# Kernel optimization log

Hardware: AMD Instinct MI355X
Metric: run time of the kernel (lower is better)

## Reference

```python
import jax, jax.numpy as jnp
import numpy as np
from jax import lax

DT = 0.001            # Euler step_size (forward default)
STEPS_PER_OUT = 5     # t spacing 0.005 / dt 0.001 (t grid aligned with step grid)


def setup_inputs() -> dict:
    key = jax.random.key(0)
    ks = jax.random.split(key, 6)
    B, K, C, F, H = 8192, 2, 2, 64, 64
    D = C * F
    x0 = jax.random.normal(ks[0], (B, K, C, F), dtype=jnp.float32)
    t = jnp.arange(51, dtype=jnp.float32) * 0.005  # 51 output times, aligned to dt grid
    # Kaiming-ish small init so tanh stays in a sane range over 250 Euler steps
    W1 = jax.random.normal(ks[1], (D, H), dtype=jnp.float32) / jnp.sqrt(jnp.float32(D))
    b1 = jax.random.normal(ks[2], (H,), dtype=jnp.float32) * 0.01
    W2 = jax.random.normal(ks[3], (H, D), dtype=jnp.float32) / jnp.sqrt(jnp.float32(H))
    b2 = jax.random.normal(ks[4], (D,), dtype=jnp.float32) * 0.01
    return {"x0": x0, "t": t, "W1": W1, "b1": b1, "W2": W2, "b2": b2}


def reference(x0, t, W1, b1, W2, b2):
    B, K, C, F = x0.shape
    T = t.shape[0]

    def dydt(y):  # tiny 2-layer tanh MLP derivative, y: [B, C*F]
        return jnp.tanh(y @ W1 + b1) @ W2 + b2

    def euler_substep(i, y):
        return y + DT * dydt(y)

    def interval(y, _):
        # STEPS_PER_OUT fixed Euler steps between consecutive output times
        y = lax.fori_loop(0, STEPS_PER_OUT, euler_substep, y)
        return y, y

    y0 = x0.reshape(B, K, C * F)[:, 0]            # flatten(start_dim=-2) then [:, 0]
    _, ys = lax.scan(interval, y0, None, length=T - 1)  # [T-1, B, D]
    out = jnp.concatenate([y0[None], ys], axis=0)       # [T, B, D]
    out = jnp.transpose(out, (1, 0, 2))                 # permute(1,0,2) -> [B, T, D]
    return out.reshape(B, T, C, F)                      # unflatten -> [B, T, C, F]
```

## Files before the change

### kernel.cpp

```cpp
#include <hip/hip_runtime.h>
#include <hip/hip_bf16.h>


typedef __attribute__((ext_vector_type(8))) short bf16x8;
typedef __attribute__((ext_vector_type(4))) float floatx4;

__device__ float g_w21[64 * 64 + 64];

static __device__ __forceinline__ short f2bf(float f) {
    return __builtin_bit_cast(short, (__bf16)f);
}

static __device__ __forceinline__ unsigned pack2(float a, float b) {
    unsigned short lo = __builtin_bit_cast(unsigned short, (__bf16)a);
    unsigned short hi = __builtin_bit_cast(unsigned short, (__bf16)b);
    return (unsigned)lo | ((unsigned)hi << 16);
}

static __device__ __forceinline__ float tanh_fast(float x) {
    float e = __expf(2.0f * x);
    return 1.0f - 2.0f * __builtin_amdgcn_rcpf(1.0f + e);
}

__global__ __launch_bounds__(64) void precompute_kernel(
    const float* __restrict__ W1, const float* __restrict__ W2,
    const float* __restrict__ b2)
{
    const int hout = threadIdx.x;
    const int hin  = blockIdx.x;
    float a0 = 0.f, a1 = 0.f, a2 = 0.f, a3 = 0.f;
    if (hin < 64) {
        #pragma unroll 4
        for (int d = 0; d < 128; d += 4) {
            a0 = fmaf(W2[hin * 128 + d + 0], W1[(d + 0) * 64 + hout], a0);
            a1 = fmaf(W2[hin * 128 + d + 1], W1[(d + 1) * 64 + hout], a1);
            a2 = fmaf(W2[hin * 128 + d + 2], W1[(d + 2) * 64 + hout], a2);
            a3 = fmaf(W2[hin * 128 + d + 3], W1[(d + 3) * 64 + hout], a3);
        }
        g_w21[hin * 64 + hout] = (a0 + a1) + (a2 + a3);
    } else {
        #pragma unroll 4
        for (int d = 0; d < 128; d += 4) {
            a0 = fmaf(b2[d + 0], W1[(d + 0) * 64 + hout], a0);
            a1 = fmaf(b2[d + 1], W1[(d + 1) * 64 + hout], a1);
            a2 = fmaf(b2[d + 2], W1[(d + 2) * 64 + hout], a2);
            a3 = fmaf(b2[d + 3], W1[(d + 3) * 64 + hout], a3);
        }
        g_w21[4096 + hout] = (a0 + a1) + (a2 + a3);
    }
}

__global__ __launch_bounds__(256, 1) void node_kernel(
    const float* __restrict__ x0, const float* __restrict__ W1,
    const float* __restrict__ b1, const float* __restrict__ W2,
    const float* __restrict__ b2, float* __restrict__ out)
{
    __shared__ __align__(16) unsigned short Ald[2][16 * 64];
    __shared__ __align__(16) unsigned short Sld[16 * 64];
    __shared__ __align__(16) unsigned short Yld[16 * 128];

    const int tid  = threadIdx.x;
    const int w    = tid >> 6;
    const int lane = tid & 63;
    const int n    = lane & 15;
    const int q    = lane >> 4;
    const int row  = (blockIdx.x << 4) + n;
    const int swz  = n & 7;

    bf16x8 w21f[2];
    #pragma unroll
    for (int kt = 0; kt < 2; ++kt) {
        const int m  = w * 16 + n;
        const int k0 = kt * 32 + q * 8;
        bf16x8 v;
        #pragma unroll
        for (int j = 0; j < 8; ++j) v[j] = f2bf(g_w21[(k0 + j) * 64 + m]);
        w21f[kt] = v;
    }
    bf16x8 w2f[2][2];
    #pragma unroll
    for (int i = 0; i < 2; ++i) {
        #pragma unroll
        for (int kt = 0; kt < 2; ++kt) {
            const int m  = w * 32 + i * 16 + n;
            const int k0 = kt * 32 + q * 8;
            bf16x8 v;
            #pragma unroll
            for (int j = 0; j < 8; ++j) v[j] = f2bf(W2[(k0 + j) * 128 + m]);
            w2f[i][kt] = v;
        }
    }

    floatx4 cf, b1f, b2f5[2];
    #pragma unroll
    for (int r = 0; r < 4; ++r) {
        cf[r]  = g_w21[4096 + w * 16 + q * 4 + r];
        b1f[r] = b1[w * 16 + q * 4 + r];
    }
    #pragma unroll
    for (int i = 0; i < 2; ++i)
        #pragma unroll
        for (int r = 0; r < 4; ++r)
            b2f5[i][r] = 5.0f * b2[w * 32 + i * 16 + q * 4 + r];

    floatx4 y[2];
    #pragma unroll
    for (int i = 0; i < 2; ++i)
        #pragma unroll
        for (int r = 0; r < 4; ++r)
            y[i][r] = x0[row * 256 + w * 32 + i * 16 + q * 4 + r];

    #pragma unroll
    for (int i = 0; i < 2; ++i) {
        const int j0 = 4 * w + 2 * i + (q >> 1);
        uint2 p;
        p.x = pack2(y[i][0], y[i][1]);
        p.y = pack2(y[i][2], y[i][3]);
        *reinterpret_cast<uint2*>(&Yld[n * 128 + (j0 ^ swz) * 8 + (q & 1) * 4]) = p;
        *reinterpret_cast<floatx4*>(out + row * 51 * 128 + w * 32 + i * 16 + q * 4) = y[i];
    }
    __syncthreads();

    floatx4 z = b1f;
    #pragma unroll
    for (int kt = 0; kt < 4; ++kt) {
        bf16x8 yb = __builtin_bit_cast(bf16x8, *reinterpret_cast<const uint4*>(
            &Yld[n * 128 + ((kt * 4 + q) ^ swz) * 8]));
        const int m  = w * 16 + n;
        const int k0 = kt * 32 + q * 8;
        bf16x8 w1t;
        #pragma unroll
        for (int j = 0; j < 8; ++j) w1t[j] = f2bf(W1[(k0 + j) * 64 + m]);
        z = __builtin_amdgcn_mfma_f32_16x16x32_bf16(w1t, yb, z, 0, 0, 0);
    }

    floatx4 S = {0.0f, 0.0f, 0.0f, 0.0f};

    const int awr  = n * 64 + (((2 * w + (q >> 1)) ^ swz) * 8) + (q & 1) * 4;
    const int ard0 = n * 64 + ((q ^ swz) * 8);
    const int ard1 = n * 64 + (((4 + q) ^ swz) * 8);

    for (int ti = 1; ti <= 50; ++ti) {
        #pragma unroll
        for (int ss = 0; ss < 5; ++ss) {
            const int p = ss & 1;
            float a0 = tanh_fast(z[0]);
            float a1 = tanh_fast(z[1]);
            float a2 = tanh_fast(z[2]);
            float a3 = tanh_fast(z[3]);
            S[0] += a0; S[1] += a1; S[2] += a2; S[3] += a3;
            uint2 pa;
            pa.x = pack2(a0, a1);
            pa.y = pack2(a2, a3);
            *reinterpret_cast<uint2*>(&Ald[p][awr]) = pa;
            if (ss == 4) {
                uint2 ps;
                ps.x = pack2(S[0], S[1]);
                ps.y = pack2(S[2], S[3]);
                *reinterpret_cast<uint2*>(&Sld[awr]) = ps;
            }
            __syncthreads();

            bf16x8 ab0 = __builtin_bit_cast(bf16x8,
                *reinterpret_cast<const uint4*>(&Ald[p][ard0]));
            bf16x8 ab1 = __builtin_bit_cast(bf16x8,
                *reinterpret_cast<const uint4*>(&Ald[p][ard1]));
            floatx4 acc = cf;
            acc = __builtin_amdgcn_mfma_f32_16x16x32_bf16(w21f[0], ab0, acc, 0, 0, 0);
            acc = __builtin_amdgcn_mfma_f32_16x16x32_bf16(w21f[1], ab1, acc, 0, 0, 0);
            #pragma unroll
            for (int r = 0; r < 4; ++r) z[r] = fmaf(0.001f, acc[r], z[r]);

            if (ss == 4) {
                bf16x8 sb0 = __builtin_bit_cast(bf16x8,
                    *reinterpret_cast<const uint4*>(&Sld[ard0]));
                bf16x8 sb1 = __builtin_bit_cast(bf16x8,
                    *reinterpret_cast<const uint4*>(&Sld[ard1]));
                floatx4 acc2[2] = { b2f5[0], b2f5[1] };
                #pragma unroll
                for (int i = 0; i < 2; ++i) {
                    acc2[i] = __builtin_amdgcn_mfma_f32_16x16x32_bf16(
                        w2f[i][0], sb0, acc2[i], 0, 0, 0);
                    acc2[i] = __builtin_amdgcn_mfma_f32_16x16x32_bf16(
                        w2f[i][1], sb1, acc2[i], 0, 0, 0);
                }
                #pragma unroll
                for (int i = 0; i < 2; ++i) {
                    #pragma unroll
                    for (int r = 0; r < 4; ++r)
                        y[i][r] = fmaf(0.001f, acc2[i][r], y[i][r]);
                    *reinterpret_cast<floatx4*>(
                        out + row * 51 * 128 + ti * 128 + w * 32 + i * 16 + q * 4) = y[i];
                }
                S = floatx4{0.0f, 0.0f, 0.0f, 0.0f};
                __syncthreads();
            }
        }
    }
}

extern "C" void kernel_launch(void* const* d_in, const int* in_sizes, int n_in,
                              void* d_out, int out_size, void* d_ws, size_t ws_size,
                              hipStream_t stream) {
    const float* x0 = (const float*)d_in[0];
    const float* W1 = (const float*)d_in[2];
    const float* b1 = (const float*)d_in[3];
    const float* W2 = (const float*)d_in[4];
    const float* b2 = (const float*)d_in[5];
    float* out = (float*)d_out;

    precompute_kernel<<<dim3(65), dim3(64), 0, stream>>>(W1, W2, b2);
    node_kernel<<<dim3(512), dim3(256), 0, stream>>>(x0, W1, b1, W2, b2, out);
}
```

Baseline: 262.3 us.

## Collapse each 16-row block to one wavefront to eliminate barrier synchronization

Each block of 16 batch rows is now handled by a single 64-lane wavefront instead of four, so that wave computes all four hidden-unit tiles and all eight output tiles itself. Because the activations are exchanged only within one wavefront, the per-substep __syncthreads calls are removed. W2 fragments are staged once into LDS and read from there per interval instead of being held in registers. The trade-off is 4x more serial MFMA and tanh work per wave and only 512 waves across the whole GPU, which may underuse the compute units. It also relies on LDS ordering within a single wavefront without explicit barriers.

```diff
diff --git a/kernel.cpp b/kernel.cpp
--- a/kernel.cpp
+++ b/kernel.cpp
@@ -50,151 +50,144 @@
     }
 }
 
-__global__ __launch_bounds__(256, 1) void node_kernel(
+__global__ __launch_bounds__(64) void node_kernel(
     const float* __restrict__ x0, const float* __restrict__ W1,
     const float* __restrict__ b1, const float* __restrict__ W2,
     const float* __restrict__ b2, float* __restrict__ out)
 {
-    __shared__ __align__(16) unsigned short Ald[2][16 * 64];
-    __shared__ __align__(16) unsigned short Sld[16 * 64];
-    __shared__ __align__(16) unsigned short Yld[16 * 128];
-
-    const int tid  = threadIdx.x;
-    const int w    = tid >> 6;
-    const int lane = tid & 63;
+    __shared__ __align__(16) unsigned short Trp[16 * 64];
+    __shared__ __align__(16) unsigned short W2f[16 * 64 * 8];
+    __shared__ __align__(16) float B2f[128];
+
+    const int lane = threadIdx.x;
     const int n    = lane & 15;
     const int q    = lane >> 4;
     const int row  = (blockIdx.x << 4) + n;
-    const int swz  = n & 7;
-
-    bf16x8 w21f[2];
-    #pragma unroll
-    for (int kt = 0; kt < 2; ++kt) {
-        const int m  = w * 16 + n;
-        const int k0 = kt * 32 + q * 8;
-        bf16x8 v;
-        #pragma unroll
-        for (int j = 0; j < 8; ++j) v[j] = f2bf(g_w21[(k0 + j) * 64 + m]);
-        w21f[kt] = v;
-    }
-    bf16x8 w2f[2][2];
-    #pragma unroll
-    for (int i = 0; i < 2; ++i) {
+    const int e    = n & 7;
+
+    for (int s = lane; s < 1024; s += 64) {
+        const int f  = s >> 6;
+        const int l  = s & 63;
+        const int k0 = (f & 1) * 32 + (l >> 4) * 8;
+        const int m  = (f >> 1) * 16 + (l & 15);
+        uint4 wv;
+        wv.x = pack2(W2[(k0 + 0) * 128 + m], W2[(k0 + 1) * 128 + m]);
+        wv.y = pack2(W2[(k0 + 2) * 128 + m], W2[(k0 + 3) * 128 + m]);
+        wv.z = pack2(W2[(k0 + 4) * 128 + m], W2[(k0 + 5) * 128 + m]);
+        wv.w = pack2(W2[(k0 + 6) * 128 + m], W2[(k0 + 7) * 128 + m]);
+        *reinterpret_cast<uint4*>(&W2f[s * 8]) = wv;
+    }
+    if (lane < 32) {
+        floatx4 v = *reinterpret_cast<const floatx4*>(&b2[lane * 4]);
+        floatx4 v5 = {5.f * v[0], 5.f * v[1], 5.f * v[2], 5.f * v[3]};
+        *reinterpret_cast<floatx4*>(&B2f[lane * 4]) = v5;
+    }
+
+    bf16x8 w21f[4][2];
+    floatx4 cf[4];
+    #pragma unroll
+    for (int mt = 0; mt < 4; ++mt) {
         #pragma unroll
         for (int kt = 0; kt < 2; ++kt) {
-            const int m  = w * 32 + i * 16 + n;
             const int k0 = kt * 32 + q * 8;
             bf16x8 v;
             #pragma unroll
-            for (int j = 0; j < 8; ++j) v[j] = f2bf(W2[(k0 + j) * 128 + m]);
-            w2f[i][kt] = v;
-        }
-    }
-
-    floatx4 cf, b1f, b2f5[2];
-    #pragma unroll
-    for (int r = 0; r < 4; ++r) {
-        cf[r]  = g_w21[4096 + w * 16 + q * 4 + r];
-        b1f[r] = b1[w * 16 + q * 4 + r];
-    }
-    #pragma unroll
-    for (int i = 0; i < 2; ++i)
-        #pragma unroll
-        for (int r = 0; r < 4; ++r)
-            b2f5[i][r] = 5.0f * b2[w * 32 + i * 16 + q * 4 + r];
-
-    floatx4 y[2];
-    #pragma unroll
-    for (int i = 0; i < 2; ++i)
-        #pragma unroll
-        for (int r = 0; r < 4; ++r)
-            y[i][r] = x0[row * 256 + w * 32 + i * 16 + q * 4 + r];
-
-    #pragma unroll
-    for (int i = 0; i < 2; ++i) {
-        const int j0 = 4 * w + 2 * i + (q >> 1);
-        uint2 p;
-        p.x = pack2(y[i][0], y[i][1]);
-        p.y = pack2(y[i][2], y[i][3]);
-        *reinterpret_cast<uint2*>(&Yld[n * 128 + (j0 ^ swz) * 8 + (q & 1) * 4]) = p;
-        *reinterpret_cast<floatx4*>(out + row * 51 * 128 + w * 32 + i * 16 + q * 4) = y[i];
-    }
-    __syncthreads();
-
-    floatx4 z = b1f;
+            for (int j = 0; j < 8; ++j)
+                v[j] = f2bf(g_w21[(k0 + j) * 64 + mt * 16 + n]);
+            w21f[mt][kt] = v;
+        }
+        cf[mt] = *reinterpret_cast<const floatx4*>(&g_w21[4096 + mt * 16 + q * 4]);
+    }
+
+    floatx4 y[8];
+    float* const outp = out + (size_t)row * (51 * 128);
+    #pragma unroll
+    for (int mt8 = 0; mt8 < 8; ++mt8) {
+        y[mt8] = *reinterpret_cast<const floatx4*>(&x0[row * 256 + mt8 * 16 + q * 4]);
+        *reinterpret_cast<floatx4*>(outp + mt8 * 16 + q * 4) = y[mt8];
+    }
+
+    floatx4 z[4];
+    #pragma unroll
+    for (int mt = 0; mt < 4; ++mt)
+        z[mt] = *reinterpret_cast<const floatx4*>(&b1[mt * 16 + q * 4]);
     #pragma unroll
     for (int kt = 0; kt < 4; ++kt) {
-        bf16x8 yb = __builtin_bit_cast(bf16x8, *reinterpret_cast<const uint4*>(
-            &Yld[n * 128 + ((kt * 4 + q) ^ swz) * 8]));
-        const int m  = w * 16 + n;
-        const int k0 = kt * 32 + q * 8;
-        bf16x8 w1t;
-        #pragma unroll
-        for (int j = 0; j < 8; ++j) w1t[j] = f2bf(W1[(k0 + j) * 64 + m]);
-        z = __builtin_amdgcn_mfma_f32_16x16x32_bf16(w1t, yb, z, 0, 0, 0);
-    }
-
-    floatx4 S = {0.0f, 0.0f, 0.0f, 0.0f};
-
-    const int awr  = n * 64 + (((2 * w + (q >> 1)) ^ swz) * 8) + (q & 1) * 4;
-    const int ard0 = n * 64 + ((q ^ swz) * 8);
-    const int ard1 = n * 64 + (((4 + q) ^ swz) * 8);
+        floatx4 lo = *reinterpret_cast<const floatx4*>(&x0[row * 256 + kt * 32 + q * 8]);
+        floatx4 hi = *reinterpret_cast<const floatx4*>(&x0[row * 256 + kt * 32 + q * 8 + 4]);
+        bf16x8 yb;
+        yb[0] = f2bf(lo[0]); yb[1] = f2bf(lo[1]); yb[2] = f2bf(lo[2]); yb[3] = f2bf(lo[3]);
+        yb[4] = f2bf(hi[0]); yb[5] = f2bf(hi[1]); yb[6] = f2bf(hi[2]); yb[7] = f2bf(hi[3]);
+        #pragma unroll
+        for (int mt = 0; mt < 4; ++mt) {
+            const int k0 = kt * 32 + q * 8;
+            bf16x8 wf;
+            #pragma unroll
+            for (int j = 0; j < 8; ++j)
+                wf[j] = f2bf(W1[(k0 + j) * 64 + mt * 16 + n]);
+            z[mt] = __builtin_amdgcn_mfma_f32_16x16x32_bf16(wf, yb, z[mt], 0, 0, 0);
+        }
+    }
+
+    floatx4 S[4];
+    #pragma unroll
+    for (int mt = 0; mt < 4; ++mt) S[mt] = floatx4{0.f, 0.f, 0.f, 0.f};
+
+    char* const trp = reinterpret_cast<char*>(Trp);
+    int wr[4], rd[2];
+    #pragma unroll
+    for (int mt = 0; mt < 4; ++mt)
+        wr[mt] = n * 128 + (((2 * mt + (q >> 1)) ^ e) * 16) + (q & 1) * 8;
+    rd[0] = n * 128 + ((q ^ e) * 16);
+    rd[1] = n * 128 + (((4 + q) ^ e) * 16);
 
     for (int ti = 1; ti <= 50; ++ti) {
         #pragma unroll
         for (int ss = 0; ss < 5; ++ss) {
-            const int p = ss & 1;
-            float a0 = tanh_fast(z[0]);
-            float a1 = tanh_fast(z[1]);
-            float a2 = tanh_fast(z[2]);
-            float a3 = tanh_fast(z[3]);
-            S[0] += a0; S[1] += a1; S[2] += a2; S[3] += a3;
-            uint2 pa;
-            pa.x = pack2(a0, a1);
-            pa.y = pack2(a2, a3);
-            *reinterpret_cast<uint2*>(&Ald[p][awr]) = pa;
-            if (ss == 4) {
-                uint2 ps;
-                ps.x = pack2(S[0], S[1]);
-                ps.y = pack2(S[2], S[3]);
-                *reinterpret_cast<uint2*>(&Sld[awr]) = ps;
+            #pragma unroll
+            for (int mt = 0; mt < 4; ++mt) {
+                float a0 = tanh_fast(z[mt][0]);
+                float a1 = tanh_fast(z[mt][1]);
+                float a2 = tanh_fast(z[mt][2]);
+                float a3 = tanh_fast(z[mt][3]);
+                S[mt][0] += a0; S[mt][1] += a1; S[mt][2] += a2; S[mt][3] += a3;
+                uint2 p; p.x = pack2(a0, a1); p.y = pack2(a2, a3);
+                *reinterpret_cast<uint2*>(trp + wr[mt]) = p;
             }
-            __syncthreads();
-
-            bf16x8 ab0 = __builtin_bit_cast(bf16x8,
-                *reinterpret_cast<const uint4*>(&Ald[p][ard0]));
-            bf16x8 ab1 = __builtin_bit_cast(bf16x8,
-                *reinterpret_cast<const uint4*>(&Ald[p][ard1]));
-            floatx4 acc = cf;
-            acc = __builtin_amdgcn_mfma_f32_16x16x32_bf16(w21f[0], ab0, acc, 0, 0, 0);
-            acc = __builtin_amdgcn_mfma_f32_16x16x32_bf16(w21f[1], ab1, acc, 0, 0, 0);
-            #pragma unroll
-            for (int r = 0; r < 4; ++r) z[r] = fmaf(0.001f, acc[r], z[r]);
-
-            if (ss == 4) {
-                bf16x8 sb0 = __builtin_bit_cast(bf16x8,
-                    *reinterpret_cast<const uint4*>(&Sld[ard0]));
-                bf16x8 sb1 = __builtin_bit_cast(bf16x8,
-                    *reinterpret_cast<const uint4*>(&Sld[ard1]));
-                floatx4 acc2[2] = { b2f5[0], b2f5[1] };
+            bf16x8 af0 = *reinterpret_cast<const bf16x8*>(trp + rd[0]);
+            bf16x8 af1 = *reinterpret_cast<const bf16x8*>(trp + rd[1]);
+
+            #pragma unroll
+            for (int mt = 0; mt < 4; ++mt) {
+                floatx4 acc = cf[mt];
+                acc = __builtin_amdgcn_mfma_f32_16x16x32_bf16(w21f[mt][0], af0, acc, 0, 0, 0);
+                acc = __builtin_amdgcn_mfma_f32_16x16x32_bf16(w21f[mt][1], af1, acc, 0, 0, 0);
                 #pragma unroll
-                for (int i = 0; i < 2; ++i) {
-                    acc2[i] = __builtin_amdgcn_mfma_f32_16x16x32_bf16(
-                        w2f[i][0], sb0, acc2[i], 0, 0, 0);
-                    acc2[i] = __builtin_amdgcn_mfma_f32_16x16x32_bf16(
-                        w2f[i][1], sb1, acc2[i], 0, 0, 0);
-                }
-                #pragma unroll
-                for (int i = 0; i < 2; ++i) {
-                    #pragma unroll
-                    for (int r = 0; r < 4; ++r)
-                        y[i][r] = fmaf(0.001f, acc2[i][r], y[i][r]);
-                    *reinterpret_cast<floatx4*>(
-                        out + row * 51 * 128 + ti * 128 + w * 32 + i * 16 + q * 4) = y[i];
-                }
-                S = floatx4{0.0f, 0.0f, 0.0f, 0.0f};
-                __syncthreads();
+                for (int r = 0; r < 4; ++r)
+                    z[mt][r] = fmaf(0.001f, acc[r], z[mt][r]);
             }
+        }
+
+        #pragma unroll
+        for (int mt = 0; mt < 4; ++mt) {
+            uint2 p; p.x = pack2(S[mt][0], S[mt][1]); p.y = pack2(S[mt][2], S[mt][3]);
+            *reinterpret_cast<uint2*>(trp + wr[mt]) = p;
+            S[mt] = floatx4{0.f, 0.f, 0.f, 0.f};
+        }
+        bf16x8 sf0 = *reinterpret_cast<const bf16x8*>(trp + rd[0]);
+        bf16x8 sf1 = *reinterpret_cast<const bf16x8*>(trp + rd[1]);
+        float* const o = outp + ti * 128;
+        #pragma unroll
+        for (int mt8 = 0; mt8 < 8; ++mt8) {
+            floatx4 acc = *reinterpret_cast<const floatx4*>(&B2f[mt8 * 16 + q * 4]);
+            bf16x8 wa = *reinterpret_cast<const bf16x8*>(&W2f[(mt8 * 2 + 0) * 512 + lane * 8]);
+            bf16x8 wb = *reinterpret_cast<const bf16x8*>(&W2f[(mt8 * 2 + 1) * 512 + lane * 8]);
+            acc = __builtin_amdgcn_mfma_f32_16x16x32_bf16(wa, sf0, acc, 0, 0, 0);
+            acc = __builtin_amdgcn_mfma_f32_16x16x32_bf16(wb, sf1, acc, 0, 0, 0);
+            #pragma unroll
+            for (int r = 0; r < 4; ++r)
+                y[mt8][r] = fmaf(0.001f, acc[r], y[mt8][r]);
+            *reinterpret_cast<floatx4*>(o + mt8 * 16 + q * 4) = y[mt8];
         }
     }
 }
@@ -210,5 +203,5 @@
     float* out = (float*)d_out;
 
     precompute_kernel<<<dim3(65), dim3(64), 0, stream>>>(W1, W2, b2);
-    node_kernel<<<dim3(512), dim3(256), 0, stream>>>(x0, W1, b1, W2, b2, out);
-}
+    node_kernel<<<dim3(512), dim3(64), 0, stream>>>(x0, W1, b1, W2, b2, out);
+}
```

After: 340.1 us. +29.6%, slower.
